# Kernel tuning notes

Measured on AMD Instinct MI355X. Metric: run time of the kernel, lower is better.

## Reference

```python
import jax, jax.numpy as jnp
import numpy as np

B, A, E = 16384, 8, 512


def setup_inputs() -> dict:
    key = jax.random.key(0)
    ks = jax.random.split(key, 6)
    return {
        "image_features": jax.random.normal(ks[0], (B, E), dtype=jnp.float32),
        "edge_attributes": jax.random.normal(ks[1], (B, A, E), dtype=jnp.float32),
        "linear_w": jax.random.normal(ks[2], (E, 2 * E), dtype=jnp.float32) * (1.0 / np.sqrt(2 * E)),
        "linear_b": jax.random.normal(ks[3], (E,), dtype=jnp.float32) * 0.01,
        "fwd_proj": jax.random.normal(ks[4], (A, E, E), dtype=jnp.float32) * (1.0 / np.sqrt(E)),
        "bwd_proj": jax.random.normal(ks[5], (A, E, E), dtype=jnp.float32) * (1.0 / np.sqrt(E)),
        "self_weighted": jnp.ones((1, A, 1), dtype=jnp.float32),
    }


def reference(image_features, edge_attributes, linear_w, linear_b, fwd_proj, bwd_proj, self_weighted):
    # Forward attribute GNN: broadcast src over attribute axis, concat, linear(2E->E)
    src = jnp.broadcast_to(image_features[:, None, :], edge_attributes.shape)  # [B,A,E]
    x = jnp.concatenate([src, edge_attributes], axis=-1)                       # [B,A,2E]
    agg = jnp.einsum('bak,ek->bae', x, linear_w) + linear_b                    # [B,A,E]
    attr_rep = jnp.einsum('bai,aij->baj', agg, fwd_proj)                       # [B,A,E]

    # Backward attribute GNN: per-type projection, ReLU, learned weighted sum over A
    proj = jnp.einsum('bai,aij->baj', attr_rep, bwd_proj)                      # [B,A,E]
    individuals = jnp.sum(jax.nn.relu(proj) * self_weighted, axis=1)           # [B,E]
    return attr_rep, individuals
```

## Files before the change

kernel.cpp:

```cpp
#include <hip/hip_runtime.h>
#include <cstdint>
#include <cstddef>

#define NB 16384
#define NA 8
#define NE 512
#define NK 1024
#define NN 4096

typedef __bf16 bf16x8 __attribute__((ext_vector_type(8)));
typedef float  f32x4  __attribute__((ext_vector_type(4)));
typedef uint16_t u16x8 __attribute__((ext_vector_type(8)));

__device__ __forceinline__ uint16_t cvt_bf16(float f) {
    uint32_t u = __builtin_bit_cast(uint32_t, f);
    u += 0x7fffu + ((u >> 16) & 1u);
    return (uint16_t)(u >> 16);
}

__device__ __forceinline__ int swz(int row) { return (row ^ (row >> 2)) & 3; }

__device__ __forceinline__ int cf_pos(int row, int c) {
    return ((row >> 1) << 3) + ((((row & 1) << 2) + c) ^ ((row >> 1) & 7));
}

__device__ __forceinline__ void gl_lds16(const void* g, void* l) {
    __builtin_amdgcn_global_load_lds(
        (__attribute__((address_space(1))) void*)(void*)g,
        (__attribute__((address_space(3))) void*)l, 16, 0, 0);
}

__device__ __forceinline__ void tcvt_tile(const float* __restrict__ src,
                                          uint16_t* __restrict__ dst,
                                          int R, int C, int c0, int r0, int t) {
    __shared__ float tile[32][33];
    int tx = t & 31, ty = t >> 5;
#pragma unroll
    for (int yy = 0; yy < 4; ++yy) {
        int r = ty + yy * 8;
        tile[r][tx] = src[(size_t)(r0 + r) * C + c0 + tx];
    }
    __syncthreads();
#pragma unroll
    for (int yy = 0; yy < 4; ++yy) {
        int c = ty + yy * 8;
        dst[(size_t)(c0 + c) * R + r0 + tx] = cvt_bf16(tile[tx][c]);
    }
}

__global__ __launch_bounds__(256) void k_pre(const float* __restrict__ lw,
                                             const float* __restrict__ fwd,
                                             const float* __restrict__ bwd,
                                             const float* __restrict__ img,
                                             const float* __restrict__ lb,
                                             const float* __restrict__ edge,
                                             uint16_t* __restrict__ lwT,
                                             uint16_t* __restrict__ fwdT,
                                             uint16_t* __restrict__ bwdT,
                                             uint16_t* __restrict__ imgb,
                                             float* __restrict__ bvec,
                                             uint16_t* __restrict__ edgeb) {
    int b = blockIdx.x, t = threadIdx.x;
    if (b < 512) {
        int bx = b & 31, by = b >> 5;
        tcvt_tile(lw, lwT, NE, NK, bx * 32, by * 32, t);
    } else if (b < 2560) {
        int i = b - 512;
        int mat = i >> 8, bx = i & 15, by = (i >> 4) & 15;
        tcvt_tile(fwd + (size_t)mat * NE * NE, fwdT + (size_t)mat * NE * NE,
                  NE, NE, bx * 32, by * 32, t);
    } else if (b < 4608) {
        int i = b - 2560;
        int mat = i >> 8, bx = i & 15, by = (i >> 4) & 15;
        tcvt_tile(bwd + (size_t)mat * NE * NE, bwdT + (size_t)mat * NE * NE,
                  NE, NE, bx * 32, by * 32, t);
    } else if (b < 12800) {
        int i = (b - 4608) * 256 + t;
        float4 v = ((const float4*)img)[i];
        ushort4 o;
        o.x = cvt_bf16(v.x); o.y = cvt_bf16(v.y); o.z = cvt_bf16(v.z); o.w = cvt_bf16(v.w);
        ((ushort4*)imgb)[i] = o;
    } else if (b < 12928) {
        int i = b - 12800;
        int a = i >> 4, i0 = (i & 15) * 32;
        float s0 = 0.f, s1 = 0.f;
#pragma unroll 4
        for (int k = 0; k < 32; ++k) {
            float w = lb[i0 + k];
            const float* f = fwd + ((size_t)a * NE + i0 + k) * NE;
            s0 = fmaf(w, f[t], s0);
            s1 = fmaf(w, f[t + 256], s1);
        }
        atomicAdd(&bvec[a * NE + t], s0);
        atomicAdd(&bvec[a * NE + t + 256], s1);
    } else {
        size_t i8 = (size_t)(b - 12928) * 256 + t;
        const float* sp = edge + i8 * 8;
        float4 v0 = ((const float4*)sp)[0];
        float4 v1 = ((const float4*)sp)[1];
        u16x8 o = {cvt_bf16(v0.x), cvt_bf16(v0.y), cvt_bf16(v0.z), cvt_bf16(v0.w),
                   cvt_bf16(v1.x), cvt_bf16(v1.y), cvt_bf16(v1.z), cvt_bf16(v1.w)};
        *(u16x8*)(edgeb + i8 * 8) = o;
    }
}

__global__ __launch_bounds__(256) void k_prep(const uint16_t* __restrict__ lwT,
                                              const uint16_t* __restrict__ fwdT,
                                              uint16_t* __restrict__ TMT) {
    __shared__ alignas(16) uint16_t lA[128 * 32];
    __shared__ alignas(16) uint16_t lB[128 * 32];
    int bz = blockIdx.x;
    int nt = bz & 31, mt = bz >> 5;
    int m0 = mt * 128, n0 = nt * 128;
    int t = threadIdx.x, lane = t & 63;
    int w = t >> 6, wm = w >> 1, wn = w & 1;
    int lr = lane & 15, lc = lane >> 4;
    int sl = swz(lr);
    f32x4 acc[4][4] = {};
    for (int k0 = 0; k0 < NE; k0 += 32) {
        __syncthreads();
#pragma unroll
        for (int p = 0; p < 2; ++p) {
            int idx = p * 256 + t;
            int row = idx >> 2, c16 = (idx & 3) ^ swz(row);
            gl_lds16(lwT + (size_t)(m0 + row) * NE + k0 + c16 * 8, lA + idx * 8);
            gl_lds16(fwdT + (size_t)(n0 + row) * NE + k0 + c16 * 8, lB + idx * 8);
        }
        __syncthreads();
        bf16x8 af[4], bfr[4];
#pragma unroll
        for (int i = 0; i < 4; ++i)
            af[i] = *(const bf16x8*)&lA[(wm * 64 + i * 16 + lr) * 32 + ((lc ^ sl) << 3)];
#pragma unroll
        for (int j = 0; j < 4; ++j)
            bfr[j] = *(const bf16x8*)&lB[(wn * 64 + j * 16 + lr) * 32 + ((lc ^ sl) << 3)];
#pragma unroll
        for (int i = 0; i < 4; ++i)
#pragma unroll
            for (int j = 0; j < 4; ++j)
                acc[i][j] = __builtin_amdgcn_mfma_f32_16x16x32_bf16(af[i], bfr[j], acc[i][j], 0, 0, 0);
    }
#pragma unroll
    for (int i = 0; i < 4; ++i) {
        int mb = m0 + wm * 64 + i * 16 + lc * 4;
#pragma unroll
        for (int j = 0; j < 4; ++j) {
            int n = n0 + wn * 64 + j * 16 + lr;
            ushort4 v;
            v.x = cvt_bf16(acc[i][j][0]);
            v.y = cvt_bf16(acc[i][j][1]);
            v.z = cvt_bf16(acc[i][j][2]);
            v.w = cvt_bf16(acc[i][j][3]);
            *(ushort4*)&TMT[(size_t)n * NK + mb] = v;
        }
    }
}

template<bool WB>
__global__ __launch_bounds__(512) void k_mm10(const uint16_t* __restrict__ imgb,
                                              const uint16_t* __restrict__ edgeb,
                                              const uint16_t* __restrict__ TMT,
                                              const float* __restrict__ bvec,
                                              float* __restrict__ attr,
                                              uint16_t* __restrict__ attrb) {
    __shared__ alignas(16) uint16_t lA[3][128 * 64];
    __shared__ alignas(16) uint16_t lB[3][256 * 64];
    int o = blockIdx.x;
    int a = o & 7, idx = o >> 3;
    int jt = idx & 1, mt = idx >> 1;
    int m0 = mt * 128, jb = jt * 256;
    int t = threadIdx.x, lane = t & 63;
    int w = t >> 6, wm = w >> 2, wn = w & 3;
    int lr = lane & 15, lc = lane >> 4;
    int srA[2], scA[2];
#pragma unroll
    for (int p = 0; p < 2; ++p) {
        int u = t + p * 512;
        srA[p] = u >> 3;
        scA[p] = ((u & 7) ^ (srA[p] & 7)) << 3;
    }
    int srB[4], scB[4];
#pragma unroll
    for (int p = 0; p < 4; ++p) {
        int u = t + p * 512;
        srB[p] = u >> 3;
        scB[p] = ((u & 7) ^ (srB[p] & 7)) << 3;
    }
    int arow[4], brow[4];
#pragma unroll
    for (int i = 0; i < 4; ++i) {
        arow[i] = wm * 64 + i * 16 + lr;
        brow[i] = wn * 64 + i * 16 + lr;
    }
    f32x4 acc[4][4] = {};

    auto stage = [&](int buf, int k) {
        if (k < 8) {
#pragma unroll
            for (int p = 0; p < 2; ++p)
                gl_lds16(imgb + (size_t)(m0 + srA[p]) * NE + k * 64 + scA[p],
                         &lA[buf][(t + p * 512) * 8]);
        } else {
#pragma unroll
            for (int p = 0; p < 2; ++p)
                gl_lds16(edgeb + ((size_t)(m0 + srA[p]) * NA + a) * NE + (k - 8) * 64 + scA[p],
                         &lA[buf][(t + p * 512) * 8]);
        }
#pragma unroll
        for (int p = 0; p < 4; ++p)
            gl_lds16(TMT + (size_t)(a * NE + jb + srB[p]) * NK + k * 64 + scB[p],
                     &lB[buf][(t + p * 512) * 8]);
    };
    auto compute = [&](int cur) {
        bf16x8 af[4][2], bfr[4][2];
#pragma unroll
        for (int i = 0; i < 4; ++i)
#pragma unroll
            for (int h = 0; h < 2; ++h)
                af[i][h] = *(const bf16x8*)&lA[cur][(arow[i] << 6) + ((((h << 2) + lc) ^ (arow[i] & 7)) << 3)];
#pragma unroll
        for (int j = 0; j < 4; ++j)
#pragma unroll
            for (int h = 0; h < 2; ++h)
                bfr[j][h] = *(const bf16x8*)&lB[cur][(brow[j] << 6) + ((((h << 2) + lc) ^ (brow[j] & 7)) << 3)];
        asm volatile("s_waitcnt lgkmcnt(0)" ::: "memory");
        __builtin_amdgcn_sched_barrier(0);
#pragma unroll
        for (int h = 0; h < 2; ++h)
#pragma unroll
            for (int i = 0; i < 4; ++i)
#pragma unroll
                for (int j = 0; j < 4; ++j)
                    acc[i][j] = __builtin_amdgcn_mfma_f32_16x16x32_bf16(af[i][h], bfr[j][h], acc[i][j], 0, 0, 0);
    };

    stage(0, 0);
    stage(1, 1);
    stage(2, 2);
    for (int k = 0; k < 14; ++k) {
        int cur = k % 3;
        asm volatile("s_waitcnt vmcnt(12)\n\ts_barrier" ::: "memory");
        compute(cur);
        asm volatile("s_barrier" ::: "memory");
        if (k < 13) stage(cur, k + 3);
    }
    asm volatile("s_waitcnt vmcnt(6)\n\ts_barrier" ::: "memory");
    compute(2);
    asm volatile("s_barrier" ::: "memory");
    asm volatile("s_waitcnt vmcnt(0)\n\ts_barrier" ::: "memory");
    compute(0);

#pragma unroll
    for (int j = 0; j < 4; ++j) {
        float bv = bvec[a * NE + jb + wn * 64 + j * 16 + lr];
#pragma unroll
        for (int i = 0; i < 4; ++i)
#pragma unroll
            for (int r = 0; r < 4; ++r)
                acc[i][j][r] += bv;
    }
#pragma unroll
    for (int i = 0; i < 4; ++i) {
#pragma unroll
        for (int r = 0; r < 4; ++r) {
            int bm = m0 + wm * 64 + i * 16 + lc * 4 + r;
            float* orow = attr + ((size_t)bm * NA + a) * NE + jb;
#pragma unroll
            for (int j = 0; j < 4; ++j)
                __builtin_nontemporal_store(acc[i][j][r], &orow[wn * 64 + j * 16 + lr]);
            if (WB) {
                uint16_t* brw = attrb + ((size_t)bm * NA + a) * NE + jb;
#pragma unroll
                for (int j = 0; j < 4; ++j)
                    brw[wn * 64 + j * 16 + lr] = cvt_bf16(acc[i][j][r]);
            }
        }
    }
}

template<bool WB>
__global__ __launch_bounds__(512) void k_mm4(const uint16_t* __restrict__ imgb,
                                             const float* __restrict__ edge,
                                             const uint16_t* __restrict__ TMT,
                                             const float* __restrict__ bvec,
                                             float* __restrict__ attr,
                                             uint16_t* __restrict__ attrb) {
    __shared__ alignas(16) uint16_t lA[2][128 * 32];
    __shared__ alignas(16) uint16_t lB[2][256 * 32];
    int o = blockIdx.x;
    int a = o & 7, idx = o >> 3;
    int jt = idx & 1, mt = idx >> 1;
    int m0 = mt * 128, jb = jt * 256;
    int t = threadIdx.x, lane = t & 63;
    int w = t >> 6, wm = w >> 2, wn = w & 3;
    int lr = lane & 15, lc = lane >> 4;
    int rpA = t >> 3, qA = (t & 7) ^ (rpA & 7);
    int srA = (rpA << 1) | (qA >> 2), scA = (qA & 3) << 3;
    int srB[2], scB[2];
#pragma unroll
    for (int p = 0; p < 2; ++p) {
        int u = t + p * 512;
        int rp = u >> 3, q = (u & 7) ^ (rp & 7);
        srB[p] = (rp << 1) | (q >> 2);
        scB[p] = (q & 3) << 3;
    }
    int er = t >> 2, ec = t & 3;
    int epos = cf_pos(er, ec) * 8;
    int aoff[4], boff[4];
#pragma unroll
    for (int i = 0; i < 4; ++i) {
        aoff[i] = cf_pos(wm * 64 + i * 16 + lr, lc) * 8;
        boff[i] = cf_pos(wn * 64 + i * 16 + lr, lc) * 8;
    }
    auto stage_img = [&](int buf, int s) {
        gl_lds16(imgb + (size_t)(m0 + srA) * NE + s * 32 + scA, &lA[buf][t * 8]);
    };
    auto stage_tmt = [&](int buf, int s) {
#pragma unroll
        for (int p = 0; p < 2; ++p)
            gl_lds16(TMT + (size_t)(a * NE + jb + srB[p]) * NK + s * 32 + scB[p],
                     &lB[buf][(t + p * 512) * 8]);
    };
    f32x4 acc[4][4] = {};
    stage_img(0, 0);
    stage_tmt(0, 0);
    for (int s = 0; s < 32; ++s) {
        int cur = s & 1, nb = cur ^ 1;
        __syncthreads();
        float4 e0, e1;
        bool eN = (s < 31) && (s + 1 >= 16);
        if (s < 31) {
            if (s + 1 < 16) {
                stage_img(nb, s + 1);
            } else {
                int kk = (s + 1 - 16) * 32;
                const float* sp = edge + ((size_t)(m0 + er) * NA + a) * NE + kk + ec * 8;
                e0 = ((const float4*)sp)[0];
                e1 = ((const float4*)sp)[1];
            }
            stage_tmt(nb, s + 1);
        }
        bf16x8 af[4], bfr[4];
#pragma unroll
        for (int i = 0; i < 4; ++i) af[i] = *(const bf16x8*)&lA[cur][aoff[i]];
#pragma unroll
        for (int j = 0; j < 4; ++j) bfr[j] = *(const bf16x8*)&lB[cur][boff[j]];
#pragma unroll
        for (int i = 0; i < 4; ++i)
#pragma unroll
            for (int j = 0; j < 4; ++j)
                acc[i][j] = __builtin_amdgcn_mfma_f32_16x16x32_bf16(af[i], bfr[j], acc[i][j], 0, 0, 0);
        if (eN) {
            u16x8 ov = {cvt_bf16(e0.x), cvt_bf16(e0.y), cvt_bf16(e0.z), cvt_bf16(e0.w),
                        cvt_bf16(e1.x), cvt_bf16(e1.y), cvt_bf16(e1.z), cvt_bf16(e1.w)};
            *(u16x8*)&lA[nb][epos] = ov;
        }
    }
#pragma unroll
    for (int j = 0; j < 4; ++j) {
        float bv = bvec[a * NE + jb + wn * 64 + j * 16 + lr];
#pragma unroll
        for (int i = 0; i < 4; ++i)
#pragma unroll
            for (int r = 0; r < 4; ++r)
                acc[i][j][r] += bv;
    }
#pragma unroll
    for (int i = 0; i < 4; ++i) {
#pragma unroll
        for (int r = 0; r < 4; ++r) {
            int bm = m0 + wm * 64 + i * 16 + lc * 4 + r;
            float* orow = attr + ((size_t)bm * NA + a) * NE + jb;
#pragma unroll
            for (int j = 0; j < 4; ++j)
                __builtin_nontemporal_store(acc[i][j][r], &orow[wn * 64 + j * 16 + lr]);
            if (WB) {
                uint16_t* brw = attrb + ((size_t)bm * NA + a) * NE + jb;
#pragma unroll
                for (int j = 0; j < 4; ++j)
                    brw[wn * 64 + j * 16 + lr] = cvt_bf16(acc[i][j][r]);
            }
        }
    }
}

template<bool AB>
__global__ __launch_bounds__(256) void k_ind4(const float* __restrict__ attrf,
                                              const uint16_t* __restrict__ attrb,
                                              const uint16_t* __restrict__ bwdT,
                                              const float* __restrict__ sw,
                                              float* __restrict__ ind) {
    __shared__ alignas(16) uint16_t lA[2][128 * 32];
    __shared__ alignas(16) uint16_t lB[2][128 * 32];
    int o = blockIdx.x;
    int xcd = o & 7, mt = o >> 3;
    int jt = xcd >> 1, ah = xcd & 1;
    int m0 = mt * 128, jb = jt * 128, a0 = ah * 4;
    int t = threadIdx.x, lane = t & 63;
    int w = t >> 6, wm = w >> 1, wn = w & 1;
    int lr = lane & 15, lc = lane >> 4;
    int srow[2], sc8[2];
#pragma unroll
    for (int p = 0; p < 2; ++p) {
        int u = p * 256 + t;
        int rp = u >> 3, q = (u & 7) ^ (rp & 7);
        srow[p] = (rp << 1) | (q >> 2);
        sc8[p] = (q & 3) << 3;
    }
    int erow[2], ec[2], epos[2];
#pragma unroll
    for (int p = 0; p < 2; ++p) {
        int u = p * 256 + t;
        erow[p] = u >> 2; ec[p] = u & 3;
        epos[p] = cf_pos(erow[p], ec[p]) * 8;
    }
    int aoff[4], boff[4];
#pragma unroll
    for (int i = 0; i < 4; ++i) {
        aoff[i] = cf_pos(wm * 64 + i * 16 + lr, lc) * 8;
        boff[i] = cf_pos(wn * 64 + i * 16 + lr, lc) * 8;
    }
    auto stage = [&](int buf, int s) {
        int aa = a0 + (s >> 4), kk = (s & 15) * 32;
        if (AB) {
#pragma unroll
            for (int p = 0; p < 2; ++p)
                gl_lds16(attrb + ((size_t)(m0 + srow[p]) * NA + aa) * NE + kk + sc8[p],
                         &lA[buf][(p * 256 + t) * 8]);
        } else {
#pragma unroll
            for (int p = 0; p < 2; ++p) {
                const float* sp = attrf + ((size_t)(m0 + erow[p]) * NA + aa) * NE + kk + ec[p] * 8;
                float4 v0 = ((const float4*)sp)[0];
                float4 v1 = ((const float4*)sp)[1];
                u16x8 ov = {cvt_bf16(v0.x), cvt_bf16(v0.y), cvt_bf16(v0.z), cvt_bf16(v0.w),
                            cvt_bf16(v1.x), cvt_bf16(v1.y), cvt_bf16(v1.z), cvt_bf16(v1.w)};
                *(u16x8*)&lA[buf][epos[p]] = ov;
            }
        }
#pragma unroll
        for (int p = 0; p < 2; ++p)
            gl_lds16(bwdT + (size_t)(aa * NE + jb + srow[p]) * NE + kk + sc8[p],
                     &lB[buf][(p * 256 + t) * 8]);
    };
    f32x4 res[4][4] = {};
    f32x4 acc[4][4] = {};
    stage(0, 0);
    for (int s = 0; s < 64; ++s) {
        int cur = s & 1;
        __syncthreads();
        if (s < 63) stage(cur ^ 1, s + 1);
        bf16x8 af[4], bfr[4];
#pragma unroll
        for (int i = 0; i < 4; ++i) af[i] = *(const bf16x8*)&lA[cur][aoff[i]];
#pragma unroll
        for (int j = 0; j < 4; ++j) bfr[j] = *(const bf16x8*)&lB[cur][boff[j]];
#pragma unroll
        for (int i = 0; i < 4; ++i)
#pragma unroll
            for (int j = 0; j < 4; ++j)
                acc[i][j] = __builtin_amdgcn_mfma_f32_16x16x32_bf16(af[i], bfr[j], acc[i][j], 0, 0, 0);
        if ((s & 15) == 15) {
            float wa = sw[a0 + (s >> 4)];
#pragma unroll
            for (int i = 0; i < 4; ++i)
#pragma unroll
                for (int j = 0; j < 4; ++j) {
#pragma unroll
                    for (int r = 0; r < 4; ++r)
                        res[i][j][r] += wa * fmaxf(acc[i][j][r], 0.f);
                    acc[i][j] = (f32x4){0.f, 0.f, 0.f, 0.f};
                }
        }
    }
#pragma unroll
    for (int i = 0; i < 4; ++i) {
#pragma unroll
        for (int r = 0; r < 4; ++r) {
            int bm = m0 + wm * 64 + i * 16 + lc * 4 + r;
            float* orow = ind + (size_t)bm * NE + jb;
#pragma unroll
            for (int j = 0; j < 4; ++j)
                atomicAdd(&orow[wn * 64 + j * 16 + lr], res[i][j][r]);
        }
    }
}

extern "C" void kernel_launch(void* const* d_in, const int* in_sizes, int n_in,
                              void* d_out, int out_size, void* d_ws, size_t ws_size,
                              hipStream_t stream) {
    (void)in_sizes; (void)n_in; (void)out_size;
    const float* img  = (const float*)d_in[0];
    const float* edge = (const float*)d_in[1];
    const float* lw   = (const float*)d_in[2];
    const float* lb   = (const float*)d_in[3];
    const float* fwd  = (const float*)d_in[4];
    const float* bwd  = (const float*)d_in[5];
    const float* sw   = (const float*)d_in[6];
    float* attr = (float*)d_out;
    float* ind  = attr + (size_t)NB * NA * NE;

    char* ws = (char*)d_ws;
    size_t off = 0;
    auto alloc = [&](size_t bytes) { void* p = ws + off; off += bytes; return p; };
    uint16_t* lwT  = (uint16_t*)alloc((size_t)NK * NE * 2);
    uint16_t* fwdT = (uint16_t*)alloc((size_t)NA * NE * NE * 2);
    uint16_t* bwdT = (uint16_t*)alloc((size_t)NA * NE * NE * 2);
    uint16_t* TMT  = (uint16_t*)alloc((size_t)NN * NK * 2);
    uint16_t* imgb = (uint16_t*)alloc((size_t)NB * NE * 2);
    float*    bvec = (float*)alloc((size_t)NN * 4);

    const size_t BIGB = (size_t)NB * NA * NE * 2;
    bool has_attrb = ws_size >= off + BIGB;
    uint16_t* attrb = has_attrb ? (uint16_t*)alloc(BIGB) : (uint16_t*)0;
    bool has_edgeb = ws_size >= off + BIGB;
    uint16_t* edgeb = has_edgeb ? (uint16_t*)alloc(BIGB) : (uint16_t*)0;

    hipMemsetAsync(bvec, 0, (size_t)NN * 4, stream);
    hipMemsetAsync(ind, 0, (size_t)NB * NE * 4, stream);

    int pre_grid = has_edgeb ? 45696 : 12928;
    k_pre<<<pre_grid, 256, 0, stream>>>(lw, fwd, bwd, img, lb, edge,
                                        lwT, fwdT, bwdT, imgb, bvec, edgeb);
    k_prep<<<(NK / 128) * (NN / 128), 256, 0, stream>>>(lwT, fwdT, TMT);

    int mm_grid = 8 * 2 * (NB / 128);
    int ind_grid = (NB / 128) * (NE / 128) * 2;

    if (has_edgeb) {
        if (has_attrb)
            k_mm10<true><<<mm_grid, 512, 0, stream>>>(imgb, edgeb, TMT, bvec, attr, attrb);
        else
            k_mm10<false><<<mm_grid, 512, 0, stream>>>(imgb, edgeb, TMT, bvec, attr, attrb);
    } else {
        if (has_attrb)
            k_mm4<true><<<mm_grid, 512, 0, stream>>>(imgb, edge, TMT, bvec, attr, attrb);
        else
            k_mm4<false><<<mm_grid, 512, 0, stream>>>(imgb, edge, TMT, bvec, attr, attrb);
    }
    if (has_attrb)
        k_ind4<true><<<ind_grid, 256, 0, stream>>>(attr, attrb, bwdT, sw, ind);
    else
        k_ind4<false><<<ind_grid, 256, 0, stream>>>(attr, attrb, bwdT, sw, ind);
}
```

Measured before the change: 450.0 us.

## Add 512-thread triple-buffered bf16 MFMA kernel for backward projection reduction

```diff
diff --git a/kernel.cpp b/kernel.cpp
--- a/kernel.cpp
+++ b/kernel.cpp
@@ -278,6 +278,123 @@
     }
 }
 
+__global__ __launch_bounds__(512) void k_ind6(const uint16_t* __restrict__ attrb,
+                                              const uint16_t* __restrict__ bwdT,
+                                              const float* __restrict__ sw,
+                                              float* __restrict__ ind) {
+    __shared__ alignas(16) uint16_t lA[3][128 * 64];
+    __shared__ alignas(16) uint16_t lB[3][256 * 64];
+    int o = blockIdx.x;
+    int xcd = o & 7;
+    int jt = xcd & 1, ah = (xcd >> 1) & 1, mtl = xcd >> 2;
+    int mt = ((o >> 3) << 1) | mtl;
+    int m0 = mt * 128, jb = jt * 256, a0 = ah * 4;
+    int t = threadIdx.x, lane = t & 63;
+    int w = t >> 6, wm = w >> 2, wn = w & 3;
+    int lr = lane & 15, lc = lane >> 4;
+    int srA[2], scA[2];
+#pragma unroll
+    for (int p = 0; p < 2; ++p) {
+        int u = t + p * 512;
+        srA[p] = u >> 3;
+        scA[p] = ((u & 7) ^ (srA[p] & 7)) << 3;
+    }
+    int srB[4], scB[4];
+#pragma unroll
+    for (int p = 0; p < 4; ++p) {
+        int u = t + p * 512;
+        srB[p] = u >> 3;
+        scB[p] = ((u & 7) ^ (srB[p] & 7)) << 3;
+    }
+    int arow[4], brow[4];
+#pragma unroll
+    for (int i = 0; i < 4; ++i) {
+        arow[i] = wm * 64 + i * 16 + lr;
+        brow[i] = wn * 64 + i * 16 + lr;
+    }
+    float w0 = sw[a0], w1 = sw[a0 + 1], w2 = sw[a0 + 2], w3 = sw[a0 + 3];
+    asm volatile("s_waitcnt vmcnt(0) lgkmcnt(0)" ::: "memory");
+
+    f32x4 acc[4][4] = {};
+    f32x4 res[4][4] = {};
+
+    auto stage = [&](int buf, int kt) {
+        int aa = a0 + (kt >> 3), kk = (kt & 7) * 64;
+#pragma unroll
+        for (int p = 0; p < 2; ++p)
+            gl_lds16(attrb + ((size_t)(m0 + srA[p]) * NA + aa) * NE + kk + scA[p],
+                     &lA[buf][(t + p * 512) * 8]);
+#pragma unroll
+        for (int p = 0; p < 4; ++p)
+            gl_lds16(bwdT + ((size_t)aa * NE + jb + srB[p]) * NE + kk + scB[p],
+                     &lB[buf][(t + p * 512) * 8]);
+    };
+    auto compute = [&](int cur) {
+        bf16x8 af[4][2], bfr[4][2];
+#pragma unroll
+        for (int i = 0; i < 4; ++i)
+#pragma unroll
+            for (int h = 0; h < 2; ++h)
+                af[i][h] = *(const bf16x8*)&lA[cur][(arow[i] << 6) + ((((h << 2) + lc) ^ (arow[i] & 7)) << 3)];
+#pragma unroll
+        for (int j = 0; j < 4; ++j)
+#pragma unroll
+            for (int h = 0; h < 2; ++h)
+                bfr[j][h] = *(const bf16x8*)&lB[cur][(brow[j] << 6) + ((((h << 2) + lc) ^ (brow[j] & 7)) << 3)];
+        asm volatile("s_waitcnt lgkmcnt(0)" ::: "memory");
+        __builtin_amdgcn_sched_barrier(0);
+#pragma unroll
+        for (int h = 0; h < 2; ++h)
+#pragma unroll
+            for (int i = 0; i < 4; ++i)
+#pragma unroll
+                for (int j = 0; j < 4; ++j)
+                    acc[i][j] = __builtin_amdgcn_mfma_f32_16x16x32_bf16(af[i][h], bfr[j][h], acc[i][j], 0, 0, 0);
+    };
+    auto finish_a = [&](int q) {
+        float wa = (q == 0) ? w0 : (q == 1) ? w1 : (q == 2) ? w2 : w3;
+#pragma unroll
+        for (int i = 0; i < 4; ++i)
+#pragma unroll
+            for (int j = 0; j < 4; ++j) {
+#pragma unroll
+                for (int r = 0; r < 4; ++r)
+                    res[i][j][r] += wa * fmaxf(acc[i][j][r], 0.f);
+                acc[i][j] = (f32x4){0.f, 0.f, 0.f, 0.f};
+            }
+    };
+
+    stage(0, 0);
+    stage(1, 1);
+    stage(2, 2);
+    for (int k = 0; k < 30; ++k) {
+        int cur = k % 3;
+        asm volatile("s_waitcnt vmcnt(12)\n\ts_barrier" ::: "memory");
+        compute(cur);
+        if ((k & 7) == 7) finish_a(k >> 3);
+        asm volatile("s_barrier" ::: "memory");
+        if (k < 29) stage(cur, k + 3);
+    }
+    asm volatile("s_waitcnt vmcnt(6)\n\ts_barrier" ::: "memory");
+    compute(0);
+    asm volatile("s_barrier" ::: "memory");
+    asm volatile("s_waitcnt vmcnt(0)\n\ts_barrier" ::: "memory");
+    compute(1);
+    finish_a(3);
+
+#pragma unroll
+    for (int i = 0; i < 4; ++i) {
+#pragma unroll
+        for (int r = 0; r < 4; ++r) {
+            int bm = m0 + wm * 64 + i * 16 + lc * 4 + r;
+            float* orow = ind + (size_t)bm * NE + jb;
+#pragma unroll
+            for (int j = 0; j < 4; ++j)
+                atomicAdd(&orow[wn * 64 + j * 16 + lr], res[i][j][r]);
+        }
+    }
+}
+
 template<bool WB>
 __global__ __launch_bounds__(512) void k_mm4(const uint16_t* __restrict__ imgb,
                                              const float* __restrict__ edge,
@@ -525,7 +642,6 @@
     k_prep<<<(NK / 128) * (NN / 128), 256, 0, stream>>>(lwT, fwdT, TMT);
 
     int mm_grid = 8 * 2 * (NB / 128);
-    int ind_grid = (NB / 128) * (NE / 128) * 2;
 
     if (has_edgeb) {
         if (has_attrb)
@@ -538,8 +654,10 @@
         else
             k_mm4<false><<<mm_grid, 512, 0, stream>>>(imgb, edge, TMT, bvec, attr, attrb);
     }
-    if (has_attrb)
-        k_ind4<true><<<ind_grid, 256, 0, stream>>>(attr, attrb, bwdT, sw, ind);
-    else
+    if (has_attrb) {
+        k_ind6<<<8 * (NB / 256), 512, 0, stream>>>(attrb, bwdT, sw, ind);
+    } else {
+        int ind_grid = (NB / 128) * (NE / 128) * 2;
         k_ind4<false><<<ind_grid, 256, 0, stream>>>(attr, attrb, bwdT, sw, ind);
-}
+    }
+}
```

New measurement: 451.7 us. No clear change (+0.4%).

## Fuse edge bf16 conversion into main GEMM and rewrite individuals kernel

Applied to the files above, without the earlier changes.

```diff
diff --git a/kernel.cpp b/kernel.cpp
--- a/kernel.cpp
+++ b/kernel.cpp
@@ -53,13 +53,11 @@
                                              const float* __restrict__ bwd,
                                              const float* __restrict__ img,
                                              const float* __restrict__ lb,
-                                             const float* __restrict__ edge,
                                              uint16_t* __restrict__ lwT,
                                              uint16_t* __restrict__ fwdT,
                                              uint16_t* __restrict__ bwdT,
                                              uint16_t* __restrict__ imgb,
-                                             float* __restrict__ bvec,
-                                             uint16_t* __restrict__ edgeb) {
+                                             float* __restrict__ bvec) {
     int b = blockIdx.x, t = threadIdx.x;
     if (b < 512) {
         int bx = b & 31, by = b >> 5;
@@ -80,7 +78,7 @@
         ushort4 o;
         o.x = cvt_bf16(v.x); o.y = cvt_bf16(v.y); o.z = cvt_bf16(v.z); o.w = cvt_bf16(v.w);
         ((ushort4*)imgb)[i] = o;
-    } else if (b < 12928) {
+    } else {
         int i = b - 12800;
         int a = i >> 4, i0 = (i & 15) * 32;
         float s0 = 0.f, s1 = 0.f;
@@ -93,14 +91,6 @@
         }
         atomicAdd(&bvec[a * NE + t], s0);
         atomicAdd(&bvec[a * NE + t + 256], s1);
-    } else {
-        size_t i8 = (size_t)(b - 12928) * 256 + t;
-        const float* sp = edge + i8 * 8;
-        float4 v0 = ((const float4*)sp)[0];
-        float4 v1 = ((const float4*)sp)[1];
-        u16x8 o = {cvt_bf16(v0.x), cvt_bf16(v0.y), cvt_bf16(v0.z), cvt_bf16(v0.w),
-                   cvt_bf16(v1.x), cvt_bf16(v1.y), cvt_bf16(v1.z), cvt_bf16(v1.w)};
-        *(u16x8*)(edgeb + i8 * 8) = o;
     }
 }
 
@@ -157,8 +147,8 @@
 }
 
 template<bool WB>
-__global__ __launch_bounds__(512) void k_mm10(const uint16_t* __restrict__ imgb,
-                                              const uint16_t* __restrict__ edgeb,
+__global__ __launch_bounds__(512) void k_mm12(const uint16_t* __restrict__ imgb,
+                                              const float* __restrict__ edge,
                                               const uint16_t* __restrict__ TMT,
                                               const float* __restrict__ bvec,
                                               float* __restrict__ attr,
@@ -186,6 +176,13 @@
         srB[p] = u >> 3;
         scB[p] = ((u & 7) ^ (srB[p] & 7)) << 3;
     }
+    int erw[2], ecn[2], eoff[2];
+#pragma unroll
+    for (int p = 0; p < 2; ++p) {
+        int u = t + p * 512;
+        erw[p] = u >> 3; ecn[p] = u & 7;
+        eoff[p] = (erw[p] << 6) + ((ecn[p] ^ (erw[p] & 7)) << 3);
+    }
     int arow[4], brow[4];
 #pragma unroll
     for (int i = 0; i < 4; ++i) {
@@ -193,22 +190,167 @@
         brow[i] = wn * 64 + i * 16 + lr;
     }
     f32x4 acc[4][4] = {};
-
-    auto stage = [&](int buf, int k) {
-        if (k < 8) {
-#pragma unroll
-            for (int p = 0; p < 2; ++p)
-                gl_lds16(imgb + (size_t)(m0 + srA[p]) * NE + k * 64 + scA[p],
-                         &lA[buf][(t + p * 512) * 8]);
-        } else {
-#pragma unroll
-            for (int p = 0; p < 2; ++p)
-                gl_lds16(edgeb + ((size_t)(m0 + srA[p]) * NA + a) * NE + (k - 8) * 64 + scA[p],
-                         &lA[buf][(t + p * 512) * 8]);
-        }
+    float4 e0[4], e1[4], e2[4];
+
+#define STAGE_B(BUF, T)                                                                 \
+    { _Pragma("unroll")                                                                 \
+      for (int p = 0; p < 4; ++p)                                                       \
+          gl_lds16(TMT + (size_t)(a * NE + jb + srB[p]) * NK + (T) * 64 + scB[p],       \
+                   &lB[BUF][(t + p * 512) * 8]); }
+#define STAGE_IMG(BUF, T)                                                               \
+    { _Pragma("unroll")                                                                 \
+      for (int p = 0; p < 2; ++p)                                                       \
+          gl_lds16(imgb + (size_t)(m0 + srA[p]) * NE + (T) * 64 + scA[p],               \
+                   &lA[BUF][(t + p * 512) * 8]);                                        \
+      STAGE_B(BUF, T) }
+#define STAGE_EDGE(BUF, T, E)                                                           \
+    { _Pragma("unroll")                                                                 \
+      for (int p = 0; p < 2; ++p) {                                                     \
+          const float* sp_ = edge + ((size_t)(m0 + erw[p]) * NA + a) * NE               \
+                             + ((T) - 8) * 64 + ecn[p] * 8;                             \
+          E[2 * p]     = ((const float4*)sp_)[0];                                       \
+          E[2 * p + 1] = ((const float4*)sp_)[1];                                       \
+      }                                                                                 \
+      STAGE_B(BUF, T) }
+#define WRITE_A(BUF, E)                                                                 \
+    { _Pragma("unroll")                                                                 \
+      for (int p = 0; p < 2; ++p) {                                                     \
+          u16x8 ov_ = {cvt_bf16(E[2*p].x),   cvt_bf16(E[2*p].y),                        \
+                       cvt_bf16(E[2*p].z),   cvt_bf16(E[2*p].w),                        \
+                       cvt_bf16(E[2*p+1].x), cvt_bf16(E[2*p+1].y),                      \
+                       cvt_bf16(E[2*p+1].z), cvt_bf16(E[2*p+1].w)};                     \
+          *(u16x8*)&lA[BUF][eoff[p]] = ov_;                                             \
+      } }
+#define WAITV(N)  asm volatile("s_waitcnt vmcnt(" #N ")" ::: "memory")
+#define BARX      asm volatile("s_barrier" ::: "memory")
+#define LGKM0     asm volatile("s_waitcnt lgkmcnt(0)" ::: "memory")
+#define COMP(CUR)                                                                       \
+    { bf16x8 af[4][2], bfr[4][2];                                                       \
+      _Pragma("unroll")                                                                 \
+      for (int i = 0; i < 4; ++i)                                                       \
+          _Pragma("unroll")                                                             \
+          for (int h = 0; h < 2; ++h)                                                   \
+              af[i][h] = *(const bf16x8*)&lA[CUR][(arow[i] << 6)                        \
+                          + ((((h << 2) + lc) ^ (arow[i] & 7)) << 3)];                  \
+      _Pragma("unroll")                                                                 \
+      for (int j = 0; j < 4; ++j)                                                       \
+          _Pragma("unroll")                                                             \
+          for (int h = 0; h < 2; ++h)                                                   \
+              bfr[j][h] = *(const bf16x8*)&lB[CUR][(brow[j] << 6)                       \
+                          + ((((h << 2) + lc) ^ (brow[j] & 7)) << 3)];                  \
+      LGKM0; __builtin_amdgcn_sched_barrier(0);                                         \
+      _Pragma("unroll")                                                                 \
+      for (int h = 0; h < 2; ++h)                                                       \
+          _Pragma("unroll")                                                             \
+          for (int i = 0; i < 4; ++i)                                                   \
+              _Pragma("unroll")                                                         \
+              for (int j = 0; j < 4; ++j)                                               \
+                  acc[i][j] = __builtin_amdgcn_mfma_f32_16x16x32_bf16(af[i][h], bfr[j][h], acc[i][j], 0, 0, 0); }
+
+    STAGE_IMG(0, 0) STAGE_IMG(1, 1) STAGE_IMG(2, 2)
+    WAITV(12); BARX; COMP(0) BARX; STAGE_IMG(0, 3)
+    WAITV(12); BARX; COMP(1) BARX; STAGE_IMG(1, 4)
+    WAITV(12); BARX; COMP(2) BARX; STAGE_IMG(2, 5)
+    WAITV(12); BARX; COMP(0) BARX; STAGE_IMG(0, 6)
+    WAITV(12); BARX; COMP(1) BARX; STAGE_IMG(1, 7)
+    WAITV(12); BARX; COMP(2) BARX; STAGE_EDGE(2, 8, e2)
+    WAITV(14); BARX; COMP(0) BARX; STAGE_EDGE(0, 9, e0)
+    WAITV(16); BARX; COMP(1) BARX; STAGE_EDGE(1, 10, e1)
+    WAITV(16); WRITE_A(2, e2) LGKM0; BARX; COMP(2) BARX; STAGE_EDGE(2, 11, e2)
+    WAITV(16); WRITE_A(0, e0) LGKM0; BARX; COMP(0) BARX; STAGE_EDGE(0, 12, e0)
+    WAITV(16); WRITE_A(1, e1) LGKM0; BARX; COMP(1) BARX; STAGE_EDGE(1, 13, e1)
+    WAITV(16); WRITE_A(2, e2) LGKM0; BARX; COMP(2) BARX; STAGE_EDGE(2, 14, e2)
+    WAITV(16); WRITE_A(0, e0) LGKM0; BARX; COMP(0) BARX; STAGE_EDGE(0, 15, e0)
+    WAITV(16); WRITE_A(1, e1) LGKM0; BARX; COMP(1) BARX;
+    WAITV(8);  WRITE_A(2, e2) LGKM0; BARX; COMP(2) BARX;
+    WAITV(0);  WRITE_A(0, e0) LGKM0; BARX; COMP(0)
+
+#undef STAGE_B
+#undef STAGE_IMG
+#undef STAGE_EDGE
+#undef WRITE_A
+#undef WAITV
+#undef BARX
+#undef LGKM0
+#undef COMP
+
+#pragma unroll
+    for (int j = 0; j < 4; ++j) {
+        float bv = bvec[a * NE + jb + wn * 64 + j * 16 + lr];
+#pragma unroll
+        for (int i = 0; i < 4; ++i)
+#pragma unroll
+            for (int r = 0; r < 4; ++r)
+                acc[i][j][r] += bv;
+    }
+#pragma unroll
+    for (int i = 0; i < 4; ++i) {
+#pragma unroll
+        for (int r = 0; r < 4; ++r) {
+            int bm = m0 + wm * 64 + i * 16 + lc * 4 + r;
+            float* orow = attr + ((size_t)bm * NA + a) * NE + jb;
+#pragma unroll
+            for (int j = 0; j < 4; ++j)
+                __builtin_nontemporal_store(acc[i][j][r], &orow[wn * 64 + j * 16 + lr]);
+            if (WB) {
+                uint16_t* brw = attrb + ((size_t)bm * NA + a) * NE + jb;
+#pragma unroll
+                for (int j = 0; j < 4; ++j)
+                    brw[wn * 64 + j * 16 + lr] = cvt_bf16(acc[i][j][r]);
+            }
+        }
+    }
+}
+
+__global__ __launch_bounds__(512) void k_ind6(const uint16_t* __restrict__ attrb,
+                                              const uint16_t* __restrict__ bwdT,
+                                              const float* __restrict__ sw,
+                                              float* __restrict__ ind) {
+    __shared__ alignas(16) uint16_t lA[3][128 * 64];
+    __shared__ alignas(16) uint16_t lB[3][256 * 64];
+    int o = blockIdx.x;
+    int xcd = o & 7;
+    int jt = xcd & 1, ah = (xcd >> 1) & 1, mtl = xcd >> 2;
+    int mt = ((o >> 3) << 1) | mtl;
+    int m0 = mt * 128, jb = jt * 256, a0 = ah * 4;
+    int t = threadIdx.x, lane = t & 63;
+    int w = t >> 6, wm = w >> 2, wn = w & 3;
+    int lr = lane & 15, lc = lane >> 4;
+    int srA[2], scA[2];
+#pragma unroll
+    for (int p = 0; p < 2; ++p) {
+        int u = t + p * 512;
+        srA[p] = u >> 3;
+        scA[p] = ((u & 7) ^ (srA[p] & 7)) << 3;
+    }
+    int srB[4], scB[4];
+#pragma unroll
+    for (int p = 0; p < 4; ++p) {
+        int u = t + p * 512;
+        srB[p] = u >> 3;
+        scB[p] = ((u & 7) ^ (srB[p] & 7)) << 3;
+    }
+    int arow[4], brow[4];
+#pragma unroll
+    for (int i = 0; i < 4; ++i) {
+        arow[i] = wm * 64 + i * 16 + lr;
+        brow[i] = wn * 64 + i * 16 + lr;
+    }
+    float w0 = sw[a0], w1 = sw[a0 + 1], w2 = sw[a0 + 2], w3 = sw[a0 + 3];
+    asm volatile("s_waitcnt vmcnt(0) lgkmcnt(0)" ::: "memory");
+
+    f32x4 acc[4][4] = {};
+    f32x4 res[4][4] = {};
+
+    auto stage = [&](int buf, int kt) {
+        int aa = a0 + (kt >> 3), kk = (kt & 7) * 64;
+#pragma unroll
+        for (int p = 0; p < 2; ++p)
+            gl_lds16(attrb + ((size_t)(m0 + srA[p]) * NA + aa) * NE + kk + scA[p],
+                     &lA[buf][(t + p * 512) * 8]);
 #pragma unroll
         for (int p = 0; p < 4; ++p)
-            gl_lds16(TMT + (size_t)(a * NE + jb + srB[p]) * NK + k * 64 + scB[p],
+            gl_lds16(bwdT + ((size_t)aa * NE + jb + srB[p]) * NE + kk + scB[p],
                      &lB[buf][(t + p * 512) * 8]);
     };
     auto compute = [&](int cur) {
@@ -233,163 +375,54 @@
                 for (int j = 0; j < 4; ++j)
                     acc[i][j] = __builtin_amdgcn_mfma_f32_16x16x32_bf16(af[i][h], bfr[j][h], acc[i][j], 0, 0, 0);
     };
+    auto finish_a = [&](int q) {
+        float wa = (q == 0) ? w0 : (q == 1) ? w1 : (q == 2) ? w2 : w3;
+#pragma unroll
+        for (int i = 0; i < 4; ++i)
+#pragma unroll
+            for (int j = 0; j < 4; ++j) {
+#pragma unroll
+                for (int r = 0; r < 4; ++r)
+                    res[i][j][r] += wa * fmaxf(acc[i][j][r], 0.f);
+                acc[i][j] = (f32x4){0.f, 0.f, 0.f, 0.f};
+            }
+    };
 
     stage(0, 0);
     stage(1, 1);
     stage(2, 2);
-    for (int k = 0; k < 14; ++k) {
+    for (int k = 0; k < 30; ++k) {
         int cur = k % 3;
         asm volatile("s_waitcnt vmcnt(12)\n\ts_barrier" ::: "memory");
         compute(cur);
+        if ((k & 7) == 7) finish_a(k >> 3);
         asm volatile("s_barrier" ::: "memory");
-        if (k < 13) stage(cur, k + 3);
+        if (k < 29) stage(cur, k + 3);
     }
     asm volatile("s_waitcnt vmcnt(6)\n\ts_barrier" ::: "memory");
-    compute(2);
+    compute(0);
     asm volatile("s_barrier" ::: "memory");
     asm volatile("s_waitcnt vmcnt(0)\n\ts_barrier" ::: "memory");
-    compute(0);
-
-#pragma unroll
-    for (int j = 0; j < 4; ++j) {
-        float bv = bvec[a * NE + jb + wn * 64 + j * 16 + lr];
-#pragma unroll
-        for (int i = 0; i < 4; ++i)
-#pragma unroll
-            for (int r = 0; r < 4; ++r)
-                acc[i][j][r] += bv;
-    }
+    compute(1);
+    finish_a(3);
+
 #pragma unroll
     for (int i = 0; i < 4; ++i) {
 #pragma unroll
         for (int r = 0; r < 4; ++r) {
             int bm = m0 + wm * 64 + i * 16 + lc * 4 + r;
-            float* orow = attr + ((size_t)bm * NA + a) * NE + jb;
+            float* orow = ind + (size_t)bm * NE + jb;
 #pragma unroll
             for (int j = 0; j < 4; ++j)
-                __builtin_nontemporal_store(acc[i][j][r], &orow[wn * 64 + j * 16 + lr]);
-            if (WB) {
-                uint16_t* brw = attrb + ((size_t)bm * NA + a) * NE + jb;
-#pragma unroll
-                for (int j = 0; j < 4; ++j)
-                    brw[wn * 64 + j * 16 + lr] = cvt_bf16(acc[i][j][r]);
-            }
-        }
-    }
-}
-
-template<bool WB>
-__global__ __launch_bounds__(512) void k_mm4(const uint16_t* __restrict__ imgb,
-                                             const float* __restrict__ edge,
-                                             const uint16_t* __restrict__ TMT,
-                                             const float* __restrict__ bvec,
-                                             float* __restrict__ attr,
-                                             uint16_t* __restrict__ attrb) {
-    __shared__ alignas(16) uint16_t lA[2][128 * 32];
-    __shared__ alignas(16) uint16_t lB[2][256 * 32];
-    int o = blockIdx.x;
-    int a = o & 7, idx = o >> 3;
-    int jt = idx & 1, mt = idx >> 1;
-    int m0 = mt * 128, jb = jt * 256;
-    int t = threadIdx.x, lane = t & 63;
-    int w = t >> 6, wm = w >> 2, wn = w & 3;
-    int lr = lane & 15, lc = lane >> 4;
-    int rpA = t >> 3, qA = (t & 7) ^ (rpA & 7);
-    int srA = (rpA << 1) | (qA >> 2), scA = (qA & 3) << 3;
-    int srB[2], scB[2];
-#pragma unroll
-    for (int p = 0; p < 2; ++p) {
-        int u = t + p * 512;
-        int rp = u >> 3, q = (u & 7) ^ (rp & 7);
-        srB[p] = (rp << 1) | (q >> 2);
-        scB[p] = (q & 3) << 3;
-    }
-    int er = t >> 2, ec = t & 3;
-    int epos = cf_pos(er, ec) * 8;
-    int aoff[4], boff[4];
-#pragma unroll
-    for (int i = 0; i < 4; ++i) {
-        aoff[i] = cf_pos(wm * 64 + i * 16 + lr, lc) * 8;
-        boff[i] = cf_pos(wn * 64 + i * 16 + lr, lc) * 8;
-    }
-    auto stage_img = [&](int buf, int s) {
-        gl_lds16(imgb + (size_t)(m0 + srA) * NE + s * 32 + scA, &lA[buf][t * 8]);
-    };
-    auto stage_tmt = [&](int buf, int s) {
-#pragma unroll
-        for (int p = 0; p < 2; ++p)
-            gl_lds16(TMT + (size_t)(a * NE + jb + srB[p]) * NK + s * 32 + scB[p],
-                     &lB[buf][(t + p * 512) * 8]);
-    };
-    f32x4 acc[4][4] = {};
-    stage_img(0, 0);
-    stage_tmt(0, 0);
-    for (int s = 0; s < 32; ++s) {
-        int cur = s & 1, nb = cur ^ 1;
-        __syncthreads();
-        float4 e0, e1;
-        bool eN = (s < 31) && (s + 1 >= 16);
-        if (s < 31) {
-            if (s + 1 < 16) {
-                stage_img(nb, s + 1);
-            } else {
-                int kk = (s + 1 - 16) * 32;
-                const float* sp = edge + ((size_t)(m0 + er) * NA + a) * NE + kk + ec * 8;
-                e0 = ((const float4*)sp)[0];
-                e1 = ((const float4*)sp)[1];
-            }
-            stage_tmt(nb, s + 1);
-        }
-        bf16x8 af[4], bfr[4];
-#pragma unroll
-        for (int i = 0; i < 4; ++i) af[i] = *(const bf16x8*)&lA[cur][aoff[i]];
-#pragma unroll
-        for (int j = 0; j < 4; ++j) bfr[j] = *(const bf16x8*)&lB[cur][boff[j]];
-#pragma unroll
-        for (int i = 0; i < 4; ++i)
-#pragma unroll
-            for (int j = 0; j < 4; ++j)
-                acc[i][j] = __builtin_amdgcn_mfma_f32_16x16x32_bf16(af[i], bfr[j], acc[i][j], 0, 0, 0);
-        if (eN) {
-            u16x8 ov = {cvt_bf16(e0.x), cvt_bf16(e0.y), cvt_bf16(e0.z), cvt_bf16(e0.w),
-                        cvt_bf16(e1.x), cvt_bf16(e1.y), cvt_bf16(e1.z), cvt_bf16(e1.w)};
-            *(u16x8*)&lA[nb][epos] = ov;
-        }
-    }
-#pragma unroll
-    for (int j = 0; j < 4; ++j) {
-        float bv = bvec[a * NE + jb + wn * 64 + j * 16 + lr];
-#pragma unroll
-        for (int i = 0; i < 4; ++i)
-#pragma unroll
-            for (int r = 0; r < 4; ++r)
-                acc[i][j][r] += bv;
-    }
-#pragma unroll
-    for (int i = 0; i < 4; ++i) {
-#pragma unroll
-        for (int r = 0; r < 4; ++r) {
-            int bm = m0 + wm * 64 + i * 16 + lc * 4 + r;
-            float* orow = attr + ((size_t)bm * NA + a) * NE + jb;
-#pragma unroll
-            for (int j = 0; j < 4; ++j)
-                __builtin_nontemporal_store(acc[i][j][r], &orow[wn * 64 + j * 16 + lr]);
-            if (WB) {
-                uint16_t* brw = attrb + ((size_t)bm * NA + a) * NE + jb;
-#pragma unroll
-                for (int j = 0; j < 4; ++j)
-                    brw[wn * 64 + j * 16 + lr] = cvt_bf16(acc[i][j][r]);
-            }
-        }
-    }
-}
-
-template<bool AB>
-__global__ __launch_bounds__(256) void k_ind4(const float* __restrict__ attrf,
-                                              const uint16_t* __restrict__ attrb,
-                                              const uint16_t* __restrict__ bwdT,
-                                              const float* __restrict__ sw,
-                                              float* __restrict__ ind) {
+                atomicAdd(&orow[wn * 64 + j * 16 + lr], res[i][j][r]);
+        }
+    }
+}
+
+__global__ __launch_bounds__(256) void k_ind4f(const float* __restrict__ attrf,
+                                               const uint16_t* __restrict__ bwdT,
+                                               const float* __restrict__ sw,
+                                               float* __restrict__ ind) {
     __shared__ alignas(16) uint16_t lA[2][128 * 32];
     __shared__ alignas(16) uint16_t lB[2][128 * 32];
     int o = blockIdx.x;
@@ -422,21 +455,14 @@
     }
     auto stage = [&](int buf, int s) {
         int aa = a0 + (s >> 4), kk = (s & 15) * 32;
-        if (AB) {
-#pragma unroll
-            for (int p = 0; p < 2; ++p)
-                gl_lds16(attrb + ((size_t)(m0 + srow[p]) * NA + aa) * NE + kk + sc8[p],
-                         &lA[buf][(p * 256 + t) * 8]);
-        } else {
-#pragma unroll
-            for (int p = 0; p < 2; ++p) {
-                const float* sp = attrf + ((size_t)(m0 + erow[p]) * NA + aa) * NE + kk + ec[p] * 8;
-                float4 v0 = ((const float4*)sp)[0];
-                float4 v1 = ((const float4*)sp)[1];
-                u16x8 ov = {cvt_bf16(v0.x), cvt_bf16(v0.y), cvt_bf16(v0.z), cvt_bf16(v0.w),
-                            cvt_bf16(v1.x), cvt_bf16(v1.y), cvt_bf16(v1.z), cvt_bf16(v1.w)};
-                *(u16x8*)&lA[buf][epos[p]] = ov;
-            }
+#pragma unroll
+        for (int p = 0; p < 2; ++p) {
+            const float* sp = attrf + ((size_t)(m0 + erow[p]) * NA + aa) * NE + kk + ec[p] * 8;
+            float4 v0 = ((const float4*)sp)[0];
+            float4 v1 = ((const float4*)sp)[1];
+            u16x8 ov = {cvt_bf16(v0.x), cvt_bf16(v0.y), cvt_bf16(v0.z), cvt_bf16(v0.w),
+                        cvt_bf16(v1.x), cvt_bf16(v1.y), cvt_bf16(v1.z), cvt_bf16(v1.w)};
+            *(u16x8*)&lA[buf][epos[p]] = ov;
         }
 #pragma unroll
         for (int p = 0; p < 2; ++p)
@@ -513,33 +539,21 @@
     const size_t BIGB = (size_t)NB * NA * NE * 2;
     bool has_attrb = ws_size >= off + BIGB;
     uint16_t* attrb = has_attrb ? (uint16_t*)alloc(BIGB) : (uint16_t*)0;
-    bool has_edgeb = ws_size >= off + BIGB;
-    uint16_t* edgeb = has_edgeb ? (uint16_t*)alloc(BIGB) : (uint16_t*)0;
 
     hipMemsetAsync(bvec, 0, (size_t)NN * 4, stream);
     hipMemsetAsync(ind, 0, (size_t)NB * NE * 4, stream);
 
-    int pre_grid = has_edgeb ? 45696 : 12928;
-    k_pre<<<pre_grid, 256, 0, stream>>>(lw, fwd, bwd, img, lb, edge,
-                                        lwT, fwdT, bwdT, imgb, bvec, edgeb);
+    k_pre<<<12928, 256, 0, stream>>>(lw, fwd, bwd, img, lb, lwT, fwdT, bwdT, imgb, bvec);
     k_prep<<<(NK / 128) * (NN / 128), 256, 0, stream>>>(lwT, fwdT, TMT);
 
     int mm_grid = 8 * 2 * (NB / 128);
-    int ind_grid = (NB / 128) * (NE / 128) * 2;
-
-    if (has_edgeb) {
-        if (has_attrb)
-            k_mm10<true><<<mm_grid, 512, 0, stream>>>(imgb, edgeb, TMT, bvec, attr, attrb);
-        else
-            k_mm10<false><<<mm_grid, 512, 0, stream>>>(imgb, edgeb, TMT, bvec, attr, attrb);
+
+    if (has_attrb) {
+        k_mm12<true><<<mm_grid, 512, 0, stream>>>(imgb, edge, TMT, bvec, attr, attrb);
+        k_ind6<<<8 * (NB / 256), 512, 0, stream>>>(attrb, bwdT, sw, ind);
     } else {
-        if (has_attrb)
-            k_mm4<true><<<mm_grid, 512, 0, stream>>>(imgb, edge, TMT, bvec, attr, attrb);
-        else
-            k_mm4<false><<<mm_grid, 512, 0, stream>>>(imgb, edge, TMT, bvec, attr, attrb);
-    }
-    if (has_attrb)
-        k_ind4<true><<<ind_grid, 256, 0, stream>>>(attr, attrb, bwdT, sw, ind);
-    else
-        k_ind4<false><<<ind_grid, 256, 0, stream>>>(attr, attrb, bwdT, sw, ind);
-}
+        k_mm12<false><<<mm_grid, 512, 0, stream>>>(imgb, edge, TMT, bvec, attr, attrb);
+        int ind_grid = (NB / 128) * (NE / 128) * 2;
+        k_ind4f<<<ind_grid, 256, 0, stream>>>(attr, bwdT, sw, ind);
+    }
+}
```

New measurement: 439.9 us. -2.2%, faster.
